# Kernel optimization log

Measured on AMD Instinct MI355X. Metric: run time of the kernel, lower is better.

Reference implementation:

```python
import jax, jax.numpy as jnp
import numpy as np

EPS = 1e-5


def _conv_w(x, k):
    # cross-correlation along width, kernel size 2, padding 1 -> width W+1
    xp = jnp.pad(x, ((0, 0), (0, 0), (0, 0), (1, 1)))
    return k[0] * xp[..., :-1] + k[1] * xp[..., 1:]


def _conv_h(x, k):
    # cross-correlation along height, kernel size 2, padding 1 -> height H+1
    xp = jnp.pad(x, ((0, 0), (0, 0), (1, 1), (0, 0)))
    return k[0] * xp[..., :-1, :] + k[1] * xp[..., 1:, :]


def _dwt(x, lp, hp):
    L = _conv_h(_conv_w(x, lp), lp)
    Hc = _conv_h(_conv_w(x, hp), hp)
    return L[:, :, ::2, ::2], Hc[:, :, ::2, ::2]


def _bn(y, g, b, m, v):
    # eval-mode batchnorm over channel axis 1
    scale = (g / jnp.sqrt(v + EPS))[None, :, None, None]
    shift = (b - m * g / jnp.sqrt(v + EPS))[None, :, None, None]
    return y * scale + shift


def setup_inputs() -> dict:
    key = jax.random.key(0)
    ks = jax.random.split(key, 8)
    S, B, H, W, C = 5, 8, 512, 512, 64
    x = jax.random.normal(ks[0], (B, 1, H, W), dtype=jnp.float32)
    lp = jnp.tile(jnp.array([0.7071, 0.7071], dtype=jnp.float32), (S, 1))
    hp = jnp.tile(jnp.array([0.7071, -0.7071], dtype=jnp.float32), (S, 1))
    w1 = jax.random.normal(ks[1], (S, C, 1), dtype=jnp.float32) * 0.5
    w2 = jax.random.normal(ks[2], (S, C, C), dtype=jnp.float32) * (1.0 / np.sqrt(C))
    g1 = jnp.ones((S, C), jnp.float32)
    b1 = jnp.zeros((S, C), jnp.float32)
    m1 = jax.random.normal(ks[3], (S, C), dtype=jnp.float32) * 0.1
    v1 = jax.random.uniform(ks[4], (S, C), dtype=jnp.float32) + 0.5
    g2 = jnp.ones((S, C), jnp.float32)
    b2 = jnp.zeros((S, C), jnp.float32)
    m2 = jax.random.normal(ks[5], (S, C), dtype=jnp.float32) * 0.1
    v2 = jax.random.uniform(ks[6], (S, C), dtype=jnp.float32) + 0.5
    return dict(x=x, lp=lp, hp=hp, w1=w1, w2=w2, g1=g1, b1=b1, m1=m1, v1=v1,
                g2=g2, b2=b2, m2=m2, v2=v2)


def reference(x, lp, hp, w1, w2, g1, b1, m1, v1, g2, b2, m2, v2):
    # Returns stacked-over-scale (L, H_coeff, processed_L):
    #   L, Hc: [S, B, 1, H', W'];  P: [S, B, 64, H', W']
    def per_scale(lp_s, hp_s, w1_s, g1_s, b1_s, m1_s, v1_s,
                  w2_s, g2_s, b2_s, m2_s, v2_s):
        L, Hc = _dwt(x, lp_s, hp_s)
        y = jnp.einsum('oc,bchw->bohw', w1_s, L)
        y = jax.nn.relu(_bn(y, g1_s, b1_s, m1_s, v1_s))
        y = jnp.einsum('oc,bchw->bohw', w2_s, y)
        y = jax.nn.relu(_bn(y, g2_s, b2_s, m2_s, v2_s))
        return L, Hc, y

    return jax.vmap(per_scale)(lp, hp, w1, g1, b1, m1, v1, w2, g2, b2, m2, v2)
```

## Files before the change

kernel.cpp:

```cpp
#include <hip/hip_runtime.h>
#include <math.h>

#define EPSF 1e-5f

constexpr int Sn = 5, Bn = 8, Hin = 512, Win = 512, Cn = 64;
constexpr int HO = 257, WO = 257;
constexpr int HW = HO * WO;
constexpr int NPIX = Bn * HW;
constexpr int TOTPIX = Sn * NPIX;

constexpr int WSF = 64 + Cn * 66 * 2;

typedef float f32x4 __attribute__((ext_vector_type(4)));

__global__ __launch_bounds__(64) void precompute_kernel(
    const float* __restrict__ w1, const float* __restrict__ w2,
    const float* __restrict__ g1, const float* __restrict__ b1,
    const float* __restrict__ m1, const float* __restrict__ v1,
    const float* __restrict__ g2, const float* __restrict__ b2,
    const float* __restrict__ m2, const float* __restrict__ v2,
    float* __restrict__ ws) {
    int s = blockIdx.x;
    int c = threadIdx.x;
    __shared__ float sa1[Cn], st1[Cn], stc[Cn], stS[Cn];
    __shared__ int   scS[Cn];

    int idx = s * Cn + c;
    float sc1 = g1[idx] / sqrtf(v1[idx] + EPSF);
    float a1  = sc1 * w1[idx];
    float t1  = b1[idx] - m1[idx] * sc1;
    sa1[c] = a1;
    st1[c] = t1;
    float tc = (a1 != 0.f) ? (-t1 / a1) : INFINITY;
    stc[c] = tc;
    __syncthreads();

    int rk = 0;
    for (int c2 = 0; c2 < Cn; c2++) {
        float t = stc[c2];
        rk += (t < tc) || (t == tc && c2 < c);
    }
    stS[rk] = tc;
    scS[rk] = c;
    __syncthreads();

    float* wss = ws + (size_t)s * WSF;
    wss[c] = stS[c];

    int o = c;
    float sc2 = g2[idx] / sqrtf(v2[idx] + EPSF);
    float t2o = b2[idx] - m2[idx] * sc2;
    const float* w2row = w2 + ((size_t)s * Cn + o) * Cn;

    float alpha = 0.f, beta = t2o;
    for (int cc = 0; cc < Cn; cc++) {
        float a = sa1[cc];
        bool act = (a < 0.f) || (a == 0.f && st1[cc] > 0.f);
        if (act) {
            float wf = sc2 * w2row[cc];
            alpha = fmaf(wf, a, alpha);
            beta  = fmaf(wf, st1[cc], beta);
        }
    }
    float2* abrow = (float2*)(wss + Cn);
    abrow[o * 66 + 0] = make_float2(alpha, beta);

    for (int r = 1; r <= Cn; r++) {
        int cc = scS[r - 1];
        float a = sa1[cc];
        if (a != 0.f) {
            float wf = sc2 * w2row[cc];
            float sgn = (a > 0.f) ? 1.f : -1.f;
            alpha = fmaf(sgn * wf, a, alpha);
            beta  = fmaf(sgn * wf, st1[cc], beta);
        }
        abrow[o * 66 + r] = make_float2(alpha, beta);
    }
}

constexpr int GPT = 4;
constexpr int TPB = 256;
constexpr int PIXPB = TPB * GPT;
constexpr int NCHUNK = (HW + PIXPB - 1) / PIXPB;

__device__ __forceinline__ float pwl(const float2 ab, float v) {
    return fmaxf(fmaf(ab.x, v, ab.y), 0.f);
}

__device__ __forceinline__ void dwt_one(
    const float* __restrict__ xb, int i, int j,
    float l0, float l1, float h0, float h1,
    const float* __restrict__ stS_,
    float& Lq, float& Hq, int& lo_out) {
    const int r0 = 2 * i - 1, r1 = 2 * i;
    const int c0 = 2 * j - 1, c1 = 2 * j;
    const float x00 = (r0 >= 0 && r0 < Hin && c0 >= 0 ) ? xb[r0 * Win + c0] : 0.f;
    const float x01 = (r0 >= 0 && r0 < Hin && c1 < Win) ? xb[r0 * Win + c1] : 0.f;
    const float x10 = (r1 < Hin && c0 >= 0 )            ? xb[r1 * Win + c0] : 0.f;
    const float x11 = (r1 < Hin && c1 < Win)            ? xb[r1 * Win + c1] : 0.f;
    Lq = l0 * (l0 * x00 + l1 * x01) + l1 * (l0 * x10 + l1 * x11);
    Hq = h0 * (h0 * x00 + h1 * x01) + h1 * (h0 * x10 + h1 * x11);
    int lo = 0, hi = Cn;
    while (lo < hi) {
        const int mid = (lo + hi) >> 1;
        if (stS_[mid] < Lq) lo = mid + 1; else hi = mid;
    }
    lo_out = lo;
}

__global__ __launch_bounds__(TPB, 4) void fused_kernel(
    const float* __restrict__ x,
    const float* __restrict__ lp, const float* __restrict__ hp,
    const float* __restrict__ ws,
    float* __restrict__ Lout, float* __restrict__ Hout,
    float* __restrict__ Pout) {
    __shared__ float  stS[Cn];
    __shared__ float2 sab[Cn * 66];

    const int tid = threadIdx.x;
    const int b = blockIdx.y, s = blockIdx.z;
    const float* wss = ws + (size_t)s * WSF;
    if (tid < Cn) stS[tid] = wss[tid];
    const float2* abg = (const float2*)(wss + Cn);
    for (int t = tid; t < Cn * 66; t += TPB) sab[t] = abg[t];
    __syncthreads();

    const float l0 = lp[2 * s], l1 = lp[2 * s + 1];
    const float h0 = hp[2 * s], h1 = hp[2 * s + 1];
    const float* xb = x + (size_t)b * (Hin * Win);

    const int pbase = (blockIdx.x * TPB + tid) * GPT;

    float Lv[GPT + 3];
    float Hv[GPT + 3];
    int   lo7[GPT + 3];

    int i = pbase / WO;
    int j = pbase - i * WO;
    #pragma unroll
    for (int q = 0; q < GPT; ++q) {
        dwt_one(xb, i, j, l0, l1, h0, h1, stS, Lv[q], Hv[q], lo7[q]);
        if (++j == WO) { j = 0; ++i; }
    }
    Lv[4] = __shfl_down(Lv[0], 1, 64);  Hv[4] = __shfl_down(Hv[0], 1, 64);
    lo7[4] = __shfl_down(lo7[0], 1, 64);
    Lv[5] = __shfl_down(Lv[1], 1, 64);  Hv[5] = __shfl_down(Hv[1], 1, 64);
    lo7[5] = __shfl_down(lo7[1], 1, 64);
    Lv[6] = __shfl_down(Lv[2], 1, 64);  Hv[6] = __shfl_down(Hv[2], 1, 64);
    lo7[6] = __shfl_down(lo7[2], 1, 64);
    if ((tid & 63) == 63) {
        #pragma unroll
        for (int q = GPT; q < GPT + 3; ++q) {
            dwt_one(xb, i, j, l0, l1, h0, h1, stS, Lv[q], Hv[q], lo7[q]);
            if (++j == WO) { j = 0; ++i; }
        }
    }

    const int sb = s * Bn + b;
    const bool fast = (pbase + GPT + 3 <= HW);

    {
        const size_t lb = (size_t)sb * HW + pbase;
        const int dlt = (4 - (sb & 3)) & 3;
        if (fast) {
            f32x4 l4, h4;
            switch (dlt) {
                case 0:  l4 = f32x4{Lv[0], Lv[1], Lv[2], Lv[3]};
                         h4 = f32x4{Hv[0], Hv[1], Hv[2], Hv[3]}; break;
                case 1:  l4 = f32x4{Lv[1], Lv[2], Lv[3], Lv[4]};
                         h4 = f32x4{Hv[1], Hv[2], Hv[3], Hv[4]}; break;
                case 2:  l4 = f32x4{Lv[2], Lv[3], Lv[4], Lv[5]};
                         h4 = f32x4{Hv[2], Hv[3], Hv[4], Hv[5]}; break;
                default: l4 = f32x4{Lv[3], Lv[4], Lv[5], Lv[6]};
                         h4 = f32x4{Hv[3], Hv[4], Hv[5], Hv[6]}; break;
            }
            __builtin_nontemporal_store(l4, (f32x4*)(Lout + lb + dlt));
            __builtin_nontemporal_store(h4, (f32x4*)(Hout + lb + dlt));
            if (pbase == 0) {
                if (dlt > 0) { Lout[lb + 0] = Lv[0]; Hout[lb + 0] = Hv[0]; }
                if (dlt > 1) { Lout[lb + 1] = Lv[1]; Hout[lb + 1] = Hv[1]; }
                if (dlt > 2) { Lout[lb + 2] = Lv[2]; Hout[lb + 2] = Hv[2]; }
            }
        } else {
            #pragma unroll
            for (int q = 0; q < GPT; ++q) {
                if (pbase + q < HW) {
                    Lout[lb + q] = Lv[q];
                    Hout[lb + q] = Hv[q];
                }
            }
        }
    }

    float* const Pb = Pout + ((size_t)sb * Cn) * HW + pbase;

    if (fast) {
        float* po = Pb;
        #pragma unroll 2
        for (int og = 0; og < Cn / 4; ++og, po += (size_t)4 * HW) {
            const int o = og * 4;
            {
                f32x4 v = f32x4{pwl(sab[o * 66 + lo7[0]], Lv[0]),
                                pwl(sab[o * 66 + lo7[1]], Lv[1]),
                                pwl(sab[o * 66 + lo7[2]], Lv[2]),
                                pwl(sab[o * 66 + lo7[3]], Lv[3])};
                __builtin_nontemporal_store(v, (f32x4*)po);
            }
            {
                f32x4 v = f32x4{pwl(sab[(o + 1) * 66 + lo7[3]], Lv[3]),
                                pwl(sab[(o + 1) * 66 + lo7[4]], Lv[4]),
                                pwl(sab[(o + 1) * 66 + lo7[5]], Lv[5]),
                                pwl(sab[(o + 1) * 66 + lo7[6]], Lv[6])};
                __builtin_nontemporal_store(v, (f32x4*)(po + HW + 3));
            }
            {
                f32x4 v = f32x4{pwl(sab[(o + 2) * 66 + lo7[2]], Lv[2]),
                                pwl(sab[(o + 2) * 66 + lo7[3]], Lv[3]),
                                pwl(sab[(o + 2) * 66 + lo7[4]], Lv[4]),
                                pwl(sab[(o + 2) * 66 + lo7[5]], Lv[5])};
                __builtin_nontemporal_store(v, (f32x4*)(po + 2 * (size_t)HW + 2));
            }
            {
                f32x4 v = f32x4{pwl(sab[(o + 3) * 66 + lo7[1]], Lv[1]),
                                pwl(sab[(o + 3) * 66 + lo7[2]], Lv[2]),
                                pwl(sab[(o + 3) * 66 + lo7[3]], Lv[3]),
                                pwl(sab[(o + 3) * 66 + lo7[4]], Lv[4])};
                __builtin_nontemporal_store(v, (f32x4*)(po + 3 * (size_t)HW + 1));
            }
        }
        if (pbase == 0) {
            float* ph = Pb;
            for (int o = 0; o < Cn; ++o, ph += HW) {
                const int d = (4 - (o & 3)) & 3;
                if (d > 0) ph[0] = pwl(sab[o * 66 + lo7[0]], Lv[0]);
                if (d > 1) ph[1] = pwl(sab[o * 66 + lo7[1]], Lv[1]);
                if (d > 2) ph[2] = pwl(sab[o * 66 + lo7[2]], Lv[2]);
            }
        }
    } else {
        #pragma unroll
        for (int q = 0; q < GPT; ++q) {
            const int px = pbase + q;
            if (px >= HW) break;
            const float Lq = Lv[q];
            const int   r  = lo7[q];
            float* Pp = Pb + q;
            #pragma unroll 8
            for (int o = 0; o < Cn; ++o) {
                Pp[(size_t)o * HW] = pwl(sab[o * 66 + r], Lq);
            }
        }
    }
}

extern "C" void kernel_launch(void* const* d_in, const int* in_sizes, int n_in,
                              void* d_out, int out_size, void* d_ws, size_t ws_size,
                              hipStream_t stream) {
    const float* x  = (const float*)d_in[0];
    const float* lp = (const float*)d_in[1];
    const float* hp = (const float*)d_in[2];
    const float* w1 = (const float*)d_in[3];
    const float* w2 = (const float*)d_in[4];
    const float* g1 = (const float*)d_in[5];
    const float* b1 = (const float*)d_in[6];
    const float* m1 = (const float*)d_in[7];
    const float* v1 = (const float*)d_in[8];
    const float* m2_unused = nullptr; (void)m2_unused;
    const float* g2 = (const float*)d_in[9];
    const float* b2 = (const float*)d_in[10];
    const float* m2 = (const float*)d_in[11];
    const float* v2 = (const float*)d_in[12];

    float* out  = (float*)d_out;
    float* Lout = out;
    float* Hout = out + TOTPIX;
    float* Pout = out + 2 * TOTPIX;
    float* ws   = (float*)d_ws;

    precompute_kernel<<<Sn, Cn, 0, stream>>>(w1, w2, g1, b1, m1, v1,
                                             g2, b2, m2, v2, ws);

    dim3 grid(NCHUNK, Bn, Sn);
    fused_kernel<<<grid, TPB, 0, stream>>>(x, lp, hp, ws, Lout, Hout, Pout);
}
```

Measured before the change: 798.8 us.

## Split fused kernel into DWT kernel and per-channel-group P store kernel

Splits the single fused kernel into a DWT kernel that writes L and H, and a second kernel that reads L back and writes the 64-channel P output in groups of four channels per block. The goal is far more, lighter blocks with a small shared-memory table, giving better occupancy and spreading the large P store over many blocks. In exchange, L is re-read from global memory once per channel group and the binary search is repeated 16 times per pixel. The P stores and the L store also drop the nontemporal hint so that L can stay cached for the re-read.

```diff
diff --git a/kernel.cpp b/kernel.cpp
--- a/kernel.cpp
+++ b/kernel.cpp
@@ -87,11 +87,10 @@
     return fmaxf(fmaf(ab.x, v, ab.y), 0.f);
 }
 
-__device__ __forceinline__ void dwt_one(
+__device__ __forceinline__ void dwt_lh(
     const float* __restrict__ xb, int i, int j,
     float l0, float l1, float h0, float h1,
-    const float* __restrict__ stS_,
-    float& Lq, float& Hq, int& lo_out) {
+    float& Lq, float& Hq) {
     const int r0 = 2 * i - 1, r1 = 2 * i;
     const int c0 = 2 * j - 1, c1 = 2 * j;
     const float x00 = (r0 >= 0 && r0 < Hin && c0 >= 0 ) ? xb[r0 * Win + c0] : 0.f;
@@ -100,30 +99,14 @@
     const float x11 = (r1 < Hin && c1 < Win)            ? xb[r1 * Win + c1] : 0.f;
     Lq = l0 * (l0 * x00 + l1 * x01) + l1 * (l0 * x10 + l1 * x11);
     Hq = h0 * (h0 * x00 + h1 * x01) + h1 * (h0 * x10 + h1 * x11);
-    int lo = 0, hi = Cn;
-    while (lo < hi) {
-        const int mid = (lo + hi) >> 1;
-        if (stS_[mid] < Lq) lo = mid + 1; else hi = mid;
-    }
-    lo_out = lo;
-}
-
-__global__ __launch_bounds__(TPB, 4) void fused_kernel(
+}
+
+__global__ __launch_bounds__(TPB) void dwt_kernel(
     const float* __restrict__ x,
     const float* __restrict__ lp, const float* __restrict__ hp,
-    const float* __restrict__ ws,
-    float* __restrict__ Lout, float* __restrict__ Hout,
-    float* __restrict__ Pout) {
-    __shared__ float  stS[Cn];
-    __shared__ float2 sab[Cn * 66];
-
+    float* __restrict__ Lout, float* __restrict__ Hout) {
     const int tid = threadIdx.x;
     const int b = blockIdx.y, s = blockIdx.z;
-    const float* wss = ws + (size_t)s * WSF;
-    if (tid < Cn) stS[tid] = wss[tid];
-    const float2* abg = (const float2*)(wss + Cn);
-    for (int t = tid; t < Cn * 66; t += TPB) sab[t] = abg[t];
-    __syncthreads();
 
     const float l0 = lp[2 * s], l1 = lp[2 * s + 1];
     const float h0 = hp[2 * s], h1 = hp[2 * s + 1];
@@ -133,122 +116,164 @@
 
     float Lv[GPT + 3];
     float Hv[GPT + 3];
-    int   lo7[GPT + 3];
 
     int i = pbase / WO;
     int j = pbase - i * WO;
     #pragma unroll
     for (int q = 0; q < GPT; ++q) {
-        dwt_one(xb, i, j, l0, l1, h0, h1, stS, Lv[q], Hv[q], lo7[q]);
+        dwt_lh(xb, i, j, l0, l1, h0, h1, Lv[q], Hv[q]);
         if (++j == WO) { j = 0; ++i; }
     }
     Lv[4] = __shfl_down(Lv[0], 1, 64);  Hv[4] = __shfl_down(Hv[0], 1, 64);
-    lo7[4] = __shfl_down(lo7[0], 1, 64);
     Lv[5] = __shfl_down(Lv[1], 1, 64);  Hv[5] = __shfl_down(Hv[1], 1, 64);
-    lo7[5] = __shfl_down(lo7[1], 1, 64);
     Lv[6] = __shfl_down(Lv[2], 1, 64);  Hv[6] = __shfl_down(Hv[2], 1, 64);
-    lo7[6] = __shfl_down(lo7[2], 1, 64);
     if ((tid & 63) == 63) {
         #pragma unroll
         for (int q = GPT; q < GPT + 3; ++q) {
-            dwt_one(xb, i, j, l0, l1, h0, h1, stS, Lv[q], Hv[q], lo7[q]);
+            dwt_lh(xb, i, j, l0, l1, h0, h1, Lv[q], Hv[q]);
             if (++j == WO) { j = 0; ++i; }
         }
     }
 
     const int sb = s * Bn + b;
+    const size_t lb = (size_t)sb * HW + pbase;
+    const int dlt = (4 - (sb & 3)) & 3;
     const bool fast = (pbase + GPT + 3 <= HW);
 
-    {
-        const size_t lb = (size_t)sb * HW + pbase;
-        const int dlt = (4 - (sb & 3)) & 3;
-        if (fast) {
-            f32x4 l4, h4;
-            switch (dlt) {
-                case 0:  l4 = f32x4{Lv[0], Lv[1], Lv[2], Lv[3]};
-                         h4 = f32x4{Hv[0], Hv[1], Hv[2], Hv[3]}; break;
-                case 1:  l4 = f32x4{Lv[1], Lv[2], Lv[3], Lv[4]};
-                         h4 = f32x4{Hv[1], Hv[2], Hv[3], Hv[4]}; break;
-                case 2:  l4 = f32x4{Lv[2], Lv[3], Lv[4], Lv[5]};
-                         h4 = f32x4{Hv[2], Hv[3], Hv[4], Hv[5]}; break;
-                default: l4 = f32x4{Lv[3], Lv[4], Lv[5], Lv[6]};
-                         h4 = f32x4{Hv[3], Hv[4], Hv[5], Hv[6]}; break;
-            }
-            __builtin_nontemporal_store(l4, (f32x4*)(Lout + lb + dlt));
-            __builtin_nontemporal_store(h4, (f32x4*)(Hout + lb + dlt));
-            if (pbase == 0) {
-                if (dlt > 0) { Lout[lb + 0] = Lv[0]; Hout[lb + 0] = Hv[0]; }
-                if (dlt > 1) { Lout[lb + 1] = Lv[1]; Hout[lb + 1] = Hv[1]; }
-                if (dlt > 2) { Lout[lb + 2] = Lv[2]; Hout[lb + 2] = Hv[2]; }
-            }
-        } else {
-            #pragma unroll
-            for (int q = 0; q < GPT; ++q) {
-                if (pbase + q < HW) {
-                    Lout[lb + q] = Lv[q];
-                    Hout[lb + q] = Hv[q];
-                }
-            }
-        }
-    }
-
-    float* const Pb = Pout + ((size_t)sb * Cn) * HW + pbase;
-
     if (fast) {
-        float* po = Pb;
-        #pragma unroll 2
-        for (int og = 0; og < Cn / 4; ++og, po += (size_t)4 * HW) {
-            const int o = og * 4;
-            {
-                f32x4 v = f32x4{pwl(sab[o * 66 + lo7[0]], Lv[0]),
-                                pwl(sab[o * 66 + lo7[1]], Lv[1]),
-                                pwl(sab[o * 66 + lo7[2]], Lv[2]),
-                                pwl(sab[o * 66 + lo7[3]], Lv[3])};
-                __builtin_nontemporal_store(v, (f32x4*)po);
-            }
-            {
-                f32x4 v = f32x4{pwl(sab[(o + 1) * 66 + lo7[3]], Lv[3]),
-                                pwl(sab[(o + 1) * 66 + lo7[4]], Lv[4]),
-                                pwl(sab[(o + 1) * 66 + lo7[5]], Lv[5]),
-                                pwl(sab[(o + 1) * 66 + lo7[6]], Lv[6])};
-                __builtin_nontemporal_store(v, (f32x4*)(po + HW + 3));
-            }
-            {
-                f32x4 v = f32x4{pwl(sab[(o + 2) * 66 + lo7[2]], Lv[2]),
-                                pwl(sab[(o + 2) * 66 + lo7[3]], Lv[3]),
-                                pwl(sab[(o + 2) * 66 + lo7[4]], Lv[4]),
-                                pwl(sab[(o + 2) * 66 + lo7[5]], Lv[5])};
-                __builtin_nontemporal_store(v, (f32x4*)(po + 2 * (size_t)HW + 2));
-            }
-            {
-                f32x4 v = f32x4{pwl(sab[(o + 3) * 66 + lo7[1]], Lv[1]),
-                                pwl(sab[(o + 3) * 66 + lo7[2]], Lv[2]),
-                                pwl(sab[(o + 3) * 66 + lo7[3]], Lv[3]),
-                                pwl(sab[(o + 3) * 66 + lo7[4]], Lv[4])};
-                __builtin_nontemporal_store(v, (f32x4*)(po + 3 * (size_t)HW + 1));
-            }
-        }
+        f32x4 l4, h4;
+        switch (dlt) {
+            case 0:  l4 = f32x4{Lv[0], Lv[1], Lv[2], Lv[3]};
+                     h4 = f32x4{Hv[0], Hv[1], Hv[2], Hv[3]}; break;
+            case 1:  l4 = f32x4{Lv[1], Lv[2], Lv[3], Lv[4]};
+                     h4 = f32x4{Hv[1], Hv[2], Hv[3], Hv[4]}; break;
+            case 2:  l4 = f32x4{Lv[2], Lv[3], Lv[4], Lv[5]};
+                     h4 = f32x4{Hv[2], Hv[3], Hv[4], Hv[5]}; break;
+            default: l4 = f32x4{Lv[3], Lv[4], Lv[5], Lv[6]};
+                     h4 = f32x4{Hv[3], Hv[4], Hv[5], Hv[6]}; break;
+        }
+        *(f32x4*)(Lout + lb + dlt) = l4;
+        __builtin_nontemporal_store(h4, (f32x4*)(Hout + lb + dlt));
         if (pbase == 0) {
-            float* ph = Pb;
-            for (int o = 0; o < Cn; ++o, ph += HW) {
-                const int d = (4 - (o & 3)) & 3;
-                if (d > 0) ph[0] = pwl(sab[o * 66 + lo7[0]], Lv[0]);
-                if (d > 1) ph[1] = pwl(sab[o * 66 + lo7[1]], Lv[1]);
-                if (d > 2) ph[2] = pwl(sab[o * 66 + lo7[2]], Lv[2]);
-            }
+            if (dlt > 0) { Lout[lb + 0] = Lv[0]; Hout[lb + 0] = Hv[0]; }
+            if (dlt > 1) { Lout[lb + 1] = Lv[1]; Hout[lb + 1] = Hv[1]; }
+            if (dlt > 2) { Lout[lb + 2] = Lv[2]; Hout[lb + 2] = Hv[2]; }
         }
     } else {
         #pragma unroll
         for (int q = 0; q < GPT; ++q) {
-            const int px = pbase + q;
+            if (pbase + q < HW) {
+                Lout[lb + q] = Lv[q];
+                Hout[lb + q] = Hv[q];
+            }
+        }
+    }
+}
+
+__global__ __launch_bounds__(TPB) void pstore_kernel(
+    const float* __restrict__ Lin,
+    const float* __restrict__ ws,
+    float* __restrict__ Pout) {
+    __shared__ float  stS[Cn];
+    __shared__ float2 sab[4 * 66];
+
+    const int tid = threadIdx.x;
+    const int og  = blockIdx.y;
+    const int sb  = blockIdx.z;
+    const int s   = sb >> 3;
+
+    const float* wss = ws + (size_t)s * WSF;
+    if (tid < Cn) stS[tid] = wss[tid];
+    const float2* abg = (const float2*)(wss + Cn) + (size_t)og * 4 * 66;
+    for (int t = tid; t < 4 * 66; t += TPB) sab[t] = abg[t];
+    __syncthreads();
+
+    const int p4 = (blockIdx.x * TPB + tid) * GPT;
+    const float* Lp = Lin + (size_t)sb * HW;
+
+    float Lv[GPT + 3];
+    int   lo7[GPT + 3];
+
+    #pragma unroll
+    for (int q = 0; q < GPT; ++q) {
+        const int px = p4 + q;
+        const float Lq = (px < HW) ? Lp[px] : 0.f;
+        Lv[q] = Lq;
+        int lo = 0, hi = Cn;
+        while (lo < hi) {
+            const int mid = (lo + hi) >> 1;
+            if (stS[mid] < Lq) lo = mid + 1; else hi = mid;
+        }
+        lo7[q] = lo;
+    }
+    Lv[4] = __shfl_down(Lv[0], 1, 64);  lo7[4] = __shfl_down(lo7[0], 1, 64);
+    Lv[5] = __shfl_down(Lv[1], 1, 64);  lo7[5] = __shfl_down(lo7[1], 1, 64);
+    Lv[6] = __shfl_down(Lv[2], 1, 64);  lo7[6] = __shfl_down(lo7[2], 1, 64);
+    if ((tid & 63) == 63) {
+        #pragma unroll
+        for (int q = GPT; q < GPT + 3; ++q) {
+            const int px = p4 + q;
+            const float Lq = (px < HW) ? Lp[px] : 0.f;
+            Lv[q] = Lq;
+            int lo = 0, hi = Cn;
+            while (lo < hi) {
+                const int mid = (lo + hi) >> 1;
+                if (stS[mid] < Lq) lo = mid + 1; else hi = mid;
+            }
+            lo7[q] = lo;
+        }
+    }
+
+    float* const Pb = Pout + ((size_t)sb * Cn + (size_t)og * 4) * HW;
+
+    if (p4 + GPT + 3 <= HW) {
+        {
+            f32x4 v = f32x4{pwl(sab[0 * 66 + lo7[0]], Lv[0]),
+                            pwl(sab[0 * 66 + lo7[1]], Lv[1]),
+                            pwl(sab[0 * 66 + lo7[2]], Lv[2]),
+                            pwl(sab[0 * 66 + lo7[3]], Lv[3])};
+            *(f32x4*)(Pb + p4) = v;
+        }
+        {
+            f32x4 v = f32x4{pwl(sab[1 * 66 + lo7[3]], Lv[3]),
+                            pwl(sab[1 * 66 + lo7[4]], Lv[4]),
+                            pwl(sab[1 * 66 + lo7[5]], Lv[5]),
+                            pwl(sab[1 * 66 + lo7[6]], Lv[6])};
+            *(f32x4*)(Pb + (size_t)HW + p4 + 3) = v;
+        }
+        {
+            f32x4 v = f32x4{pwl(sab[2 * 66 + lo7[2]], Lv[2]),
+                            pwl(sab[2 * 66 + lo7[3]], Lv[3]),
+                            pwl(sab[2 * 66 + lo7[4]], Lv[4]),
+                            pwl(sab[2 * 66 + lo7[5]], Lv[5])};
+            *(f32x4*)(Pb + 2 * (size_t)HW + p4 + 2) = v;
+        }
+        {
+            f32x4 v = f32x4{pwl(sab[3 * 66 + lo7[1]], Lv[1]),
+                            pwl(sab[3 * 66 + lo7[2]], Lv[2]),
+                            pwl(sab[3 * 66 + lo7[3]], Lv[3]),
+                            pwl(sab[3 * 66 + lo7[4]], Lv[4])};
+            *(f32x4*)(Pb + 3 * (size_t)HW + p4 + 1) = v;
+        }
+        if (p4 == 0) {
+            Pb[1 * (size_t)HW + 0] = pwl(sab[1 * 66 + lo7[0]], Lv[0]);
+            Pb[1 * (size_t)HW + 1] = pwl(sab[1 * 66 + lo7[1]], Lv[1]);
+            Pb[1 * (size_t)HW + 2] = pwl(sab[1 * 66 + lo7[2]], Lv[2]);
+            Pb[2 * (size_t)HW + 0] = pwl(sab[2 * 66 + lo7[0]], Lv[0]);
+            Pb[2 * (size_t)HW + 1] = pwl(sab[2 * 66 + lo7[1]], Lv[1]);
+            Pb[3 * (size_t)HW + 0] = pwl(sab[3 * 66 + lo7[0]], Lv[0]);
+        }
+    } else {
+        #pragma unroll
+        for (int q = 0; q < GPT; ++q) {
+            const int px = p4 + q;
             if (px >= HW) break;
             const float Lq = Lv[q];
             const int   r  = lo7[q];
-            float* Pp = Pb + q;
-            #pragma unroll 8
-            for (int o = 0; o < Cn; ++o) {
-                Pp[(size_t)o * HW] = pwl(sab[o * 66 + r], Lq);
-            }
+            Pb[0 * (size_t)HW + px] = pwl(sab[0 * 66 + r], Lq);
+            Pb[1 * (size_t)HW + px] = pwl(sab[1 * 66 + r], Lq);
+            Pb[2 * (size_t)HW + px] = pwl(sab[2 * 66 + r], Lq);
+            Pb[3 * (size_t)HW + px] = pwl(sab[3 * 66 + r], Lq);
         }
     }
 }
@@ -265,7 +290,6 @@
     const float* b1 = (const float*)d_in[6];
     const float* m1 = (const float*)d_in[7];
     const float* v1 = (const float*)d_in[8];
-    const float* m2_unused = nullptr; (void)m2_unused;
     const float* g2 = (const float*)d_in[9];
     const float* b2 = (const float*)d_in[10];
     const float* m2 = (const float*)d_in[11];
@@ -280,6 +304,9 @@
     precompute_kernel<<<Sn, Cn, 0, stream>>>(w1, w2, g1, b1, m1, v1,
                                              g2, b2, m2, v2, ws);
 
-    dim3 grid(NCHUNK, Bn, Sn);
-    fused_kernel<<<grid, TPB, 0, stream>>>(x, lp, hp, ws, Lout, Hout, Pout);
-}
+    dim3 grid1(NCHUNK, Bn, Sn);
+    dwt_kernel<<<grid1, TPB, 0, stream>>>(x, lp, hp, Lout, Hout);
+
+    dim3 grid2(NCHUNK, Cn / 4, Sn * Bn);
+    pstore_kernel<<<grid2, TPB, 0, stream>>>(Lout, ws, Pout);
+}
```

Result: no change. 798.9 us (+0.0%).
